# Optimization experiments

Hardware: AMD Instinct MI355X
Metric: run time of the kernel (lower is better)

The kernel has to match this reference:

```python
import jax, jax.numpy as jnp
import numpy as np

N, DEG, F = 500000, 16, 128
H1, H2, OUT = 256, 256, 128


def setup_inputs() -> dict:
    key = jax.random.key(0)
    ks = jax.random.split(key, 8)
    s = lambda fan_in: 1.0 / np.sqrt(fan_in)
    return {
        "message": jax.random.normal(ks[0], (N, DEG, F), dtype=jnp.float32),
        "features": jax.random.normal(ks[1], (N, F), dtype=jnp.float32),
        "global_features": jax.random.normal(ks[2], (N, F), dtype=jnp.float32),
        "W1": jax.random.normal(ks[3], (3 * F, H1), dtype=jnp.float32) * s(3 * F),
        "b1": jnp.zeros((H1,), dtype=jnp.float32),
        "W2": jax.random.normal(ks[4], (H1, H2), dtype=jnp.float32) * s(H1),
        "b2": jnp.zeros((H2,), dtype=jnp.float32),
        "W3": jax.random.normal(ks[5], (H2, OUT), dtype=jnp.float32) * s(H2),
        "b3": jnp.zeros((OUT,), dtype=jnp.float32),
    }


def reference(message, features, global_features, W1, b1, W2, b2, W3, b3):
    # mailbox sum-aggregate over neighbors: [N, deg, F] -> [N, F]
    agg = jnp.sum(message, axis=1)
    # concat aggregated messages with node + global features: [N, 3F]
    x = jnp.concatenate([agg, features, global_features], axis=1)
    # MLP: Linear+ReLU, Linear+ReLU, Linear
    h = jax.nn.relu(x @ W1 + b1)
    h = jax.nn.relu(h @ W2 + b2)
    out = h @ W3 + b3
    # row-wise L2 (Frobenius over dim=1) normalization
    norm = jnp.linalg.norm(out, axis=1, keepdims=True)
    return out / (norm + 1e-8)
```

## Files before the change

### kernel.cpp

```cpp
#include <hip/hip_runtime.h>


typedef short short8   __attribute__((ext_vector_type(8)));
typedef short short4_t __attribute__((ext_vector_type(4)));
typedef float f32x4    __attribute__((ext_vector_type(4)));

#define SWZ(row, off) ((off) ^ (((row) & 7) << 4))

__device__ __forceinline__ unsigned short f2bf(float f) {
    unsigned int u = __float_as_uint(f);
    u += 0x7fffu + ((u >> 16) & 1u);
    return (unsigned short)(u >> 16);
}

__global__ void prep_weights(const float* __restrict__ W1,
                             const float* __restrict__ W2,
                             const float* __restrict__ W3,
                             short* __restrict__ pw1,
                             short* __restrict__ pw2,
                             short* __restrict__ pw3) {
    int idx = blockIdx.x * 256 + threadIdx.x;
    if (idx < 98304) {
        int j = idx & 7, l = (idx >> 3) & 63, g = idx >> 9;
        int ks = g % 12, tn = g / 12;
        int n = tn * 16 + (l & 15);
        int k = ks * 32 + ((l >> 4) << 3) + j;
        pw1[idx] = (short)f2bf(W1[k * 256 + n]);
    } else if (idx < 98304 + 65536) {
        int e = idx - 98304;
        int j = e & 7, l = (e >> 3) & 63, g = e >> 9;
        int ks = g & 7, tn = g >> 3;
        int n = tn * 16 + (l & 15);
        int k = ks * 32 + ((l >> 4) << 3) + j;
        pw2[e] = (short)f2bf(W2[k * 256 + n]);
    } else if (idx < 98304 + 65536 + 32768) {
        int e = idx - 98304 - 65536;
        int j = e & 7, l = (e >> 3) & 63, g = e >> 9;
        int ks = g & 7, tn = g >> 3;
        int n = tn * 16 + (l & 15);
        int k = ks * 32 + ((l >> 4) << 3) + j;
        pw3[e] = (short)f2bf(W3[k * 128 + n]);
    }
}

__global__ __launch_bounds__(256, 4) void node_net_fused(
    const float* __restrict__ msg,
    const float* __restrict__ feat,
    const float* __restrict__ glob,
    const float* __restrict__ b1v,
    const float* __restrict__ b2v,
    const float* __restrict__ b3v,
    const short* __restrict__ pw1,
    const short* __restrict__ pw2,
    const short* __restrict__ pw3,
    float* __restrict__ out,
    int n_rows)
{
    __shared__ char lds[32768];
    char* regA = lds;
    char* regB = lds + 16384;

    {
        const unsigned key = ((unsigned)blockIdx.x * 2654435761u) >> 30;
        const int spin = (int)key * 500;
        for (int i = 0; i < spin; ++i)
            asm volatile("s_nop 0" ::: "memory");
    }

    const int tid  = threadIdx.x;
    const int lane = tid & 63;
    const int w    = tid >> 6;
    const int lr   = lane & 15;
    const int lk   = lane >> 4;
    const long long r0 = (long long)blockIdx.x * 32;

    const f32x4 zero4 = {0.f, 0.f, 0.f, 0.f};

    f32x4 fr[4], gr[4];
    #pragma unroll
    for (int q = 0; q < 4; ++q) {
        int r = (tid >> 5) + q * 8;
        long long row = r0 + r;
        fr[q] = zero4; gr[q] = zero4;
        if (row < n_rows) {
            fr[q] = __builtin_nontemporal_load((const f32x4*)feat + row * 32 + (tid & 31));
            gr[q] = __builtin_nontemporal_load((const f32x4*)glob + row * 32 + (tid & 31));
        }
    }

    #pragma unroll 1
    for (int pp = 0; pp < 4; ++pp) {
        const int rA = 8 * w + 2 * pp;
        const long long rowA = r0 + rA;
        const f32x4* base = (const f32x4*)msg + rowA * 512;
        f32x4 tA[8], tB[8];
        const bool okA = rowA < n_rows;
        const bool okB = (rowA + 1) < n_rows;
        #pragma unroll
        for (int i = 0; i < 8; ++i)
            tA[i] = okA ? __builtin_nontemporal_load(base + i * 64 + lane) : zero4;
        #pragma unroll
        for (int i = 0; i < 8; ++i)
            tB[i] = okB ? __builtin_nontemporal_load(base + 512 + i * 64 + lane) : zero4;
        f32x4 sA = ((tA[0]+tA[1])+(tA[2]+tA[3])) + ((tA[4]+tA[5])+(tA[6]+tA[7]));
        f32x4 sB = ((tB[0]+tB[1])+(tB[2]+tB[3])) + ((tB[4]+tB[5])+(tB[6]+tB[7]));
        #pragma unroll
        for (int c = 0; c < 4; ++c) {
            sA[c] += __shfl_xor(sA[c], 32);
            sB[c] += __shfl_xor(sB[c], 32);
        }
        f32x4 s = (lane < 32) ? sA : sB;
        short4_t s4;
        s4[0] = (short)f2bf(s[0]); s4[1] = (short)f2bf(s[1]);
        s4[2] = (short)f2bf(s[2]); s4[3] = (short)f2bf(s[3]);
        const int orow = rA + (lane >> 5);
        *(short4_t*)(regB + SWZ(orow, orow * 256 + (lane & 31) * 8)) = s4;
    }
    __syncthreads();

    #pragma unroll
    for (int q = 0; q < 4; ++q) {
        int r = (tid >> 5) + q * 8;
        short4_t s4;
        s4[0] = (short)f2bf(fr[q][0]); s4[1] = (short)f2bf(fr[q][1]);
        s4[2] = (short)f2bf(fr[q][2]); s4[3] = (short)f2bf(fr[q][3]);
        *(short4_t*)(regA + SWZ(r, r * 256 + (tid & 31) * 8)) = s4;
    }

    f32x4 acc1[2][4];
    #pragma unroll
    for (int ri = 0; ri < 2; ++ri)
        #pragma unroll
        for (int ci = 0; ci < 4; ++ci) acc1[ri][ci] = zero4;

    #pragma unroll
    for (int s = 0; s < 4; ++s) {
        short8 a[2], b[4];
        #pragma unroll
        for (int ri = 0; ri < 2; ++ri) {
            int row = ri * 16 + lr;
            a[ri] = *(const short8*)(regB + SWZ(row, row * 256 + s * 64 + lk * 16));
        }
        #pragma unroll
        for (int ci = 0; ci < 4; ++ci) {
            int tn = w * 4 + ci;
            b[ci] = *(const short8*)(pw1 + (((tn * 12 + s) * 64 + lane) << 3));
        }
        #pragma unroll
        for (int ri = 0; ri < 2; ++ri)
            #pragma unroll
            for (int ci = 0; ci < 4; ++ci)
                acc1[ri][ci] = __builtin_amdgcn_mfma_f32_16x16x32_bf16(
                    a[ri], b[ci], acc1[ri][ci], 0, 0, 0);
    }
    __syncthreads();

    #pragma unroll
    for (int q = 0; q < 4; ++q) {
        int r = (tid >> 5) + q * 8;
        short4_t s4;
        s4[0] = (short)f2bf(gr[q][0]); s4[1] = (short)f2bf(gr[q][1]);
        s4[2] = (short)f2bf(gr[q][2]); s4[3] = (short)f2bf(gr[q][3]);
        *(short4_t*)(regB + 8192 + SWZ(r, r * 256 + (tid & 31) * 8)) = s4;
    }

    #pragma unroll
    for (int s = 0; s < 4; ++s) {
        short8 a[2], b[4];
        #pragma unroll
        for (int ri = 0; ri < 2; ++ri) {
            int row = ri * 16 + lr;
            a[ri] = *(const short8*)(regA + SWZ(row, row * 256 + s * 64 + lk * 16));
        }
        #pragma unroll
        for (int ci = 0; ci < 4; ++ci) {
            int tn = w * 4 + ci;
            b[ci] = *(const short8*)(pw1 + (((tn * 12 + 4 + s) * 64 + lane) << 3));
        }
        #pragma unroll
        for (int ri = 0; ri < 2; ++ri)
            #pragma unroll
            for (int ci = 0; ci < 4; ++ci)
                acc1[ri][ci] = __builtin_amdgcn_mfma_f32_16x16x32_bf16(
                    a[ri], b[ci], acc1[ri][ci], 0, 0, 0);
    }
    __syncthreads();

    #pragma unroll
    for (int s = 0; s < 4; ++s) {
        short8 a[2], b[4];
        #pragma unroll
        for (int ri = 0; ri < 2; ++ri) {
            int row = ri * 16 + lr;
            a[ri] = *(const short8*)(regB + 8192 + SWZ(row, row * 256 + s * 64 + lk * 16));
        }
        #pragma unroll
        for (int ci = 0; ci < 4; ++ci) {
            int tn = w * 4 + ci;
            b[ci] = *(const short8*)(pw1 + (((tn * 12 + 8 + s) * 64 + lane) << 3));
        }
        #pragma unroll
        for (int ri = 0; ri < 2; ++ri)
            #pragma unroll
            for (int ci = 0; ci < 4; ++ci)
                acc1[ri][ci] = __builtin_amdgcn_mfma_f32_16x16x32_bf16(
                    a[ri], b[ci], acc1[ri][ci], 0, 0, 0);
    }

    #pragma unroll
    for (int ci = 0; ci < 4; ++ci) {
        int col = w * 64 + ci * 16 + lr;
        float bias = b1v[col];
        #pragma unroll
        for (int ri = 0; ri < 2; ++ri)
            #pragma unroll
            for (int i = 0; i < 4; ++i) {
                int row = ri * 16 + lk * 4 + i;
                float v = fmaxf(acc1[ri][ci][i] + bias, 0.f);
                *(short*)(regA + SWZ(row, row * 512 + col * 2)) = (short)f2bf(v);
            }
    }
    __syncthreads();

    f32x4 acc2[2][4];
    #pragma unroll
    for (int ri = 0; ri < 2; ++ri)
        #pragma unroll
        for (int ci = 0; ci < 4; ++ci) acc2[ri][ci] = zero4;

    #pragma unroll
    for (int s = 0; s < 8; ++s) {
        short8 a[2], b[4];
        #pragma unroll
        for (int ri = 0; ri < 2; ++ri) {
            int row = ri * 16 + lr;
            a[ri] = *(const short8*)(regA + SWZ(row, row * 512 + s * 64 + lk * 16));
        }
        #pragma unroll
        for (int ci = 0; ci < 4; ++ci) {
            int tn = w * 4 + ci;
            b[ci] = *(const short8*)(pw2 + (((tn * 8 + s) * 64 + lane) << 3));
        }
        #pragma unroll
        for (int ri = 0; ri < 2; ++ri)
            #pragma unroll
            for (int ci = 0; ci < 4; ++ci)
                acc2[ri][ci] = __builtin_amdgcn_mfma_f32_16x16x32_bf16(
                    a[ri], b[ci], acc2[ri][ci], 0, 0, 0);
    }

    #pragma unroll
    for (int ci = 0; ci < 4; ++ci) {
        int col = w * 64 + ci * 16 + lr;
        float bias = b2v[col];
        #pragma unroll
        for (int ri = 0; ri < 2; ++ri)
            #pragma unroll
            for (int i = 0; i < 4; ++i) {
                int row = ri * 16 + lk * 4 + i;
                float v = fmaxf(acc2[ri][ci][i] + bias, 0.f);
                *(short*)(regB + SWZ(row, row * 512 + col * 2)) = (short)f2bf(v);
            }
    }
    __syncthreads();

    f32x4 acc3[2][2];
    #pragma unroll
    for (int ri = 0; ri < 2; ++ri)
        #pragma unroll
        for (int ci = 0; ci < 2; ++ci) acc3[ri][ci] = zero4;

    #pragma unroll
    for (int s = 0; s < 8; ++s) {
        short8 a[2], b[2];
        #pragma unroll
        for (int ri = 0; ri < 2; ++ri) {
            int row = ri * 16 + lr;
            a[ri] = *(const short8*)(regB + SWZ(row, row * 512 + s * 64 + lk * 16));
        }
        #pragma unroll
        for (int ci = 0; ci < 2; ++ci) {
            int tn = w * 2 + ci;
            b[ci] = *(const short8*)(pw3 + (((tn * 8 + s) * 64 + lane) << 3));
        }
        #pragma unroll
        for (int ri = 0; ri < 2; ++ri)
            #pragma unroll
            for (int ci = 0; ci < 2; ++ci)
                acc3[ri][ci] = __builtin_amdgcn_mfma_f32_16x16x32_bf16(
                    a[ri], b[ci], acc3[ri][ci], 0, 0, 0);
    }

    #pragma unroll
    for (int ci = 0; ci < 2; ++ci) {
        int col = w * 32 + ci * 16 + lr;
        float bias = b3v[col];
        #pragma unroll
        for (int ri = 0; ri < 2; ++ri)
            #pragma unroll
            for (int i = 0; i < 4; ++i) {
                int row = ri * 16 + lk * 4 + i;
                float v = acc3[ri][ci][i] + bias;
                *(float*)(regA + SWZ(row, row * 512 + col * 4)) = v;
            }
    }
    __syncthreads();

    #pragma unroll
    for (int pass = 0; pass < 4; ++pass) {
        const int r  = (tid >> 5) + pass * 8;
        const int fl = tid & 31;
        f32x4 v = *(const f32x4*)(regA + SWZ(r, r * 512 + fl * 16));
        float ss = v[0]*v[0] + v[1]*v[1] + v[2]*v[2] + v[3]*v[3];
        ss += __shfl_xor(ss, 1, 32);
        ss += __shfl_xor(ss, 2, 32);
        ss += __shfl_xor(ss, 4, 32);
        ss += __shfl_xor(ss, 8, 32);
        ss += __shfl_xor(ss, 16, 32);
        float inv = 1.f / (sqrtf(ss) + 1e-8f);
        long long row = r0 + r;
        if (row < n_rows) {
            f32x4 o = v * inv;
            __builtin_nontemporal_store(o, (f32x4*)out + row * 32 + fl);
        }
    }
}

extern "C" void kernel_launch(void* const* d_in, const int* in_sizes, int n_in,
                              void* d_out, int out_size, void* d_ws, size_t ws_size,
                              hipStream_t stream) {
    const float* msg  = (const float*)d_in[0];
    const float* feat = (const float*)d_in[1];
    const float* glob = (const float*)d_in[2];
    const float* W1   = (const float*)d_in[3];
    const float* b1   = (const float*)d_in[4];
    const float* W2   = (const float*)d_in[5];
    const float* b2   = (const float*)d_in[6];
    const float* W3   = (const float*)d_in[7];
    const float* b3   = (const float*)d_in[8];
    float* out = (float*)d_out;

    const int n_rows = in_sizes[1] / 128;

    short* pw1 = (short*)d_ws;
    short* pw2 = pw1 + 98304;
    short* pw3 = pw2 + 65536;

    hipLaunchKernelGGL(prep_weights, dim3(768), dim3(256), 0, stream,
                       W1, W2, W3, pw1, pw2, pw3);

    const int nblocks = (n_rows + 31) / 32;
    hipLaunchKernelGGL(node_net_fused, dim3(nblocks), dim3(256), 0, stream,
                       msg, feat, glob, b1, b2, b3, pw1, pw2, pw3, out, n_rows);
}
```

Measured before the change: 1.119 ms.

## Warp-specialize persistent kernel: producer waves stream messages while MLP waves compute

Replaces the one-tile-per-block fused kernel with a persistent 512-thread kernel. Four waves run the three-layer MLP on the current 32-row tile while four producer waves stream and reduce the next tile's messages and features into a double-buffered LDS region. This is meant to overlap the heavy message read (about 4 GB of fp32) with MFMA work and removes the staggered spin delay. It uses more LDS (80 KB) and caps the grid at 512 blocks, which lowers occupancy and may underfill the memory pipeline, since only four waves per block issue the streaming loads.

```diff
diff --git a/kernel.cpp b/kernel.cpp
--- a/kernel.cpp
+++ b/kernel.cpp
@@ -43,7 +43,62 @@
     }
 }
 
-__global__ __launch_bounds__(256, 4) void node_net_fused(
+__device__ __forceinline__ void stream_pair(
+    const float* __restrict__ msg, char* aggdst,
+    long long rn0, int sw, int pp, int lane, int n_rows)
+{
+    const f32x4 zero4 = {0.f, 0.f, 0.f, 0.f};
+    const int rA = 8 * sw + 2 * pp;
+    const long long rowA = rn0 + rA;
+    const f32x4* base = (const f32x4*)msg + rowA * 512;
+    const bool okA = rowA < n_rows;
+    const bool okB = (rowA + 1) < n_rows;
+    f32x4 tA[8], tB[8];
+    #pragma unroll
+    for (int i = 0; i < 8; ++i)
+        tA[i] = okA ? __builtin_nontemporal_load(base + i * 64 + lane) : zero4;
+    #pragma unroll
+    for (int i = 0; i < 8; ++i)
+        tB[i] = okB ? __builtin_nontemporal_load(base + 512 + i * 64 + lane) : zero4;
+    f32x4 sA = ((tA[0]+tA[1])+(tA[2]+tA[3])) + ((tA[4]+tA[5])+(tA[6]+tA[7]));
+    f32x4 sB = ((tB[0]+tB[1])+(tB[2]+tB[3])) + ((tB[4]+tB[5])+(tB[6]+tB[7]));
+    #pragma unroll
+    for (int c = 0; c < 4; ++c) {
+        sA[c] += __shfl_xor(sA[c], 32);
+        sB[c] += __shfl_xor(sB[c], 32);
+    }
+    f32x4 s = (lane < 32) ? sA : sB;
+    short4_t s4;
+    s4[0] = (short)f2bf(s[0]); s4[1] = (short)f2bf(s[1]);
+    s4[2] = (short)f2bf(s[2]); s4[3] = (short)f2bf(s[3]);
+    const int orow = rA + (lane >> 5);
+    *(short4_t*)(aggdst + SWZ(orow, orow * 256 + (lane & 31) * 8)) = s4;
+}
+
+__device__ __forceinline__ void stream_fg(
+    const float* __restrict__ feat, const float* __restrict__ glob,
+    char* xbdst, long long rn0, int sw, int lane, int n_rows)
+{
+    const f32x4 zero4 = {0.f, 0.f, 0.f, 0.f};
+    const int rl = 8 * sw + (lane >> 3);
+    const long long grow = rn0 + rl;
+    const bool ok = grow < n_rows;
+    #pragma unroll
+    for (int q = 0; q < 4; ++q) {
+        const int f = (lane & 7) * 4 + q;
+        f32x4 fv = ok ? __builtin_nontemporal_load((const f32x4*)feat + grow * 32 + f) : zero4;
+        f32x4 gv = ok ? __builtin_nontemporal_load((const f32x4*)glob + grow * 32 + f) : zero4;
+        short4_t sf, sg;
+        sf[0]=(short)f2bf(fv[0]); sf[1]=(short)f2bf(fv[1]);
+        sf[2]=(short)f2bf(fv[2]); sf[3]=(short)f2bf(fv[3]);
+        sg[0]=(short)f2bf(gv[0]); sg[1]=(short)f2bf(gv[1]);
+        sg[2]=(short)f2bf(gv[2]); sg[3]=(short)f2bf(gv[3]);
+        *(short4_t*)(xbdst + 8192  + SWZ(rl, rl * 256 + f * 8)) = sf;
+        *(short4_t*)(xbdst + 16384 + SWZ(rl, rl * 256 + f * 8)) = sg;
+    }
+}
+
+__global__ __launch_bounds__(512, 2) void node_net_pc(
     const float* __restrict__ msg,
     const float* __restrict__ feat,
     const float* __restrict__ glob,
@@ -54,275 +109,198 @@
     const short* __restrict__ pw2,
     const short* __restrict__ pw3,
     float* __restrict__ out,
-    int n_rows)
+    int n_rows, int ntiles, int nblk)
 {
-    __shared__ char lds[32768];
-    char* regA = lds;
-    char* regB = lds + 16384;
-
-    {
-        const unsigned key = ((unsigned)blockIdx.x * 2654435761u) >> 30;
-        const int spin = (int)key * 500;
-        for (int i = 0; i < spin; ++i)
-            asm volatile("s_nop 0" ::: "memory");
-    }
+    __shared__ char lds[81920];
+    char* H1 = lds + 49152;
+    char* H2 = lds + 65536;
 
     const int tid  = threadIdx.x;
     const int lane = tid & 63;
     const int w    = tid >> 6;
+    const bool is_mlp = (w < 4);
+    const int sw   = w - 4;
     const int lr   = lane & 15;
     const int lk   = lane >> 4;
-    const long long r0 = (long long)blockIdx.x * 32;
-
     const f32x4 zero4 = {0.f, 0.f, 0.f, 0.f};
 
-    f32x4 fr[4], gr[4];
-    #pragma unroll
-    for (int q = 0; q < 4; ++q) {
-        int r = (tid >> 5) + q * 8;
-        long long row = r0 + r;
-        fr[q] = zero4; gr[q] = zero4;
-        if (row < n_rows) {
-            fr[q] = __builtin_nontemporal_load((const f32x4*)feat + row * 32 + (tid & 31));
-            gr[q] = __builtin_nontemporal_load((const f32x4*)glob + row * 32 + (tid & 31));
-        }
-    }
-
-    #pragma unroll 1
-    for (int pp = 0; pp < 4; ++pp) {
-        const int rA = 8 * w + 2 * pp;
-        const long long rowA = r0 + rA;
-        const f32x4* base = (const f32x4*)msg + rowA * 512;
-        f32x4 tA[8], tB[8];
-        const bool okA = rowA < n_rows;
-        const bool okB = (rowA + 1) < n_rows;
-        #pragma unroll
-        for (int i = 0; i < 8; ++i)
-            tA[i] = okA ? __builtin_nontemporal_load(base + i * 64 + lane) : zero4;
-        #pragma unroll
-        for (int i = 0; i < 8; ++i)
-            tB[i] = okB ? __builtin_nontemporal_load(base + 512 + i * 64 + lane) : zero4;
-        f32x4 sA = ((tA[0]+tA[1])+(tA[2]+tA[3])) + ((tA[4]+tA[5])+(tA[6]+tA[7]));
-        f32x4 sB = ((tB[0]+tB[1])+(tB[2]+tB[3])) + ((tB[4]+tB[5])+(tB[6]+tB[7]));
-        #pragma unroll
-        for (int c = 0; c < 4; ++c) {
-            sA[c] += __shfl_xor(sA[c], 32);
-            sB[c] += __shfl_xor(sB[c], 32);
-        }
-        f32x4 s = (lane < 32) ? sA : sB;
-        short4_t s4;
-        s4[0] = (short)f2bf(s[0]); s4[1] = (short)f2bf(s[1]);
-        s4[2] = (short)f2bf(s[2]); s4[3] = (short)f2bf(s[3]);
-        const int orow = rA + (lane >> 5);
-        *(short4_t*)(regB + SWZ(orow, orow * 256 + (lane & 31) * 8)) = s4;
-    }
-    __syncthreads();
-
-    #pragma unroll
-    for (int q = 0; q < 4; ++q) {
-        int r = (tid >> 5) + q * 8;
-        short4_t s4;
-        s4[0] = (short)f2bf(fr[q][0]); s4[1] = (short)f2bf(fr[q][1]);
-        s4[2] = (short)f2bf(fr[q][2]); s4[3] = (short)f2bf(fr[q][3]);
-        *(short4_t*)(regA + SWZ(r, r * 256 + (tid & 31) * 8)) = s4;
-    }
-
-    f32x4 acc1[2][4];
-    #pragma unroll
-    for (int ri = 0; ri < 2; ++ri)
-        #pragma unroll
-        for (int ci = 0; ci < 4; ++ci) acc1[ri][ci] = zero4;
-
-    #pragma unroll
-    for (int s = 0; s < 4; ++s) {
-        short8 a[2], b[4];
-        #pragma unroll
-        for (int ri = 0; ri < 2; ++ri) {
-            int row = ri * 16 + lr;
-            a[ri] = *(const short8*)(regB + SWZ(row, row * 256 + s * 64 + lk * 16));
-        }
+    float bias1[4] = {0,0,0,0}, bias2[4] = {0,0,0,0}, bias3[2] = {0,0};
+    if (is_mlp) {
         #pragma unroll
         for (int ci = 0; ci < 4; ++ci) {
-            int tn = w * 4 + ci;
-            b[ci] = *(const short8*)(pw1 + (((tn * 12 + s) * 64 + lane) << 3));
+            bias1[ci] = b1v[w * 64 + ci * 16 + lr];
+            bias2[ci] = b2v[w * 64 + ci * 16 + lr];
         }
         #pragma unroll
-        for (int ri = 0; ri < 2; ++ri)
-            #pragma unroll
-            for (int ci = 0; ci < 4; ++ci)
-                acc1[ri][ci] = __builtin_amdgcn_mfma_f32_16x16x32_bf16(
-                    a[ri], b[ci], acc1[ri][ci], 0, 0, 0);
+        for (int ci = 0; ci < 2; ++ci) bias3[ci] = b3v[w * 32 + ci * 16 + lr];
+    }
+
+    long long t = blockIdx.x;
+    int p = 0;
+
+    if (!is_mlp) {
+        const long long r0 = t * 32;
+        #pragma unroll 1
+        for (int pp = 0; pp < 4; ++pp)
+            stream_pair(msg, lds + 0, r0, sw, pp, lane, n_rows);
+        stream_fg(feat, glob, lds + 0, r0, sw, lane, n_rows);
     }
     __syncthreads();
 
-    #pragma unroll
-    for (int q = 0; q < 4; ++q) {
-        int r = (tid >> 5) + q * 8;
-        short4_t s4;
-        s4[0] = (short)f2bf(gr[q][0]); s4[1] = (short)f2bf(gr[q][1]);
-        s4[2] = (short)f2bf(gr[q][2]); s4[3] = (short)f2bf(gr[q][3]);
-        *(short4_t*)(regB + 8192 + SWZ(r, r * 256 + (tid & 31) * 8)) = s4;
-    }
-
-    #pragma unroll
-    for (int s = 0; s < 4; ++s) {
-        short8 a[2], b[4];
-        #pragma unroll
-        for (int ri = 0; ri < 2; ++ri) {
-            int row = ri * 16 + lr;
-            a[ri] = *(const short8*)(regA + SWZ(row, row * 256 + s * 64 + lk * 16));
-        }
-        #pragma unroll
-        for (int ci = 0; ci < 4; ++ci) {
-            int tn = w * 4 + ci;
-            b[ci] = *(const short8*)(pw1 + (((tn * 12 + 4 + s) * 64 + lane) << 3));
-        }
-        #pragma unroll
-        for (int ri = 0; ri < 2; ++ri)
-            #pragma unroll
-            for (int ci = 0; ci < 4; ++ci)
-                acc1[ri][ci] = __builtin_amdgcn_mfma_f32_16x16x32_bf16(
-                    a[ri], b[ci], acc1[ri][ci], 0, 0, 0);
-    }
-    __syncthreads();
-
-    #pragma unroll
-    for (int s = 0; s < 4; ++s) {
-        short8 a[2], b[4];
-        #pragma unroll
-        for (int ri = 0; ri < 2; ++ri) {
-            int row = ri * 16 + lr;
-            a[ri] = *(const short8*)(regB + 8192 + SWZ(row, row * 256 + s * 64 + lk * 16));
-        }
-        #pragma unroll
-        for (int ci = 0; ci < 4; ++ci) {
-            int tn = w * 4 + ci;
-            b[ci] = *(const short8*)(pw1 + (((tn * 12 + 8 + s) * 64 + lane) << 3));
-        }
-        #pragma unroll
-        for (int ri = 0; ri < 2; ++ri)
-            #pragma unroll
-            for (int ci = 0; ci < 4; ++ci)
-                acc1[ri][ci] = __builtin_amdgcn_mfma_f32_16x16x32_bf16(
-                    a[ri], b[ci], acc1[ri][ci], 0, 0, 0);
-    }
-
-    #pragma unroll
-    for (int ci = 0; ci < 4; ++ci) {
-        int col = w * 64 + ci * 16 + lr;
-        float bias = b1v[col];
-        #pragma unroll
-        for (int ri = 0; ri < 2; ++ri)
-            #pragma unroll
-            for (int i = 0; i < 4; ++i) {
-                int row = ri * 16 + lk * 4 + i;
-                float v = fmaxf(acc1[ri][ci][i] + bias, 0.f);
-                *(short*)(regA + SWZ(row, row * 512 + col * 2)) = (short)f2bf(v);
-            }
-    }
-    __syncthreads();
-
-    f32x4 acc2[2][4];
-    #pragma unroll
-    for (int ri = 0; ri < 2; ++ri)
-        #pragma unroll
-        for (int ci = 0; ci < 4; ++ci) acc2[ri][ci] = zero4;
-
-    #pragma unroll
-    for (int s = 0; s < 8; ++s) {
-        short8 a[2], b[4];
-        #pragma unroll
-        for (int ri = 0; ri < 2; ++ri) {
-            int row = ri * 16 + lr;
-            a[ri] = *(const short8*)(regA + SWZ(row, row * 512 + s * 64 + lk * 16));
-        }
-        #pragma unroll
-        for (int ci = 0; ci < 4; ++ci) {
-            int tn = w * 4 + ci;
-            b[ci] = *(const short8*)(pw2 + (((tn * 8 + s) * 64 + lane) << 3));
-        }
-        #pragma unroll
-        for (int ri = 0; ri < 2; ++ri)
-            #pragma unroll
-            for (int ci = 0; ci < 4; ++ci)
-                acc2[ri][ci] = __builtin_amdgcn_mfma_f32_16x16x32_bf16(
-                    a[ri], b[ci], acc2[ri][ci], 0, 0, 0);
-    }
-
-    #pragma unroll
-    for (int ci = 0; ci < 4; ++ci) {
-        int col = w * 64 + ci * 16 + lr;
-        float bias = b2v[col];
-        #pragma unroll
-        for (int ri = 0; ri < 2; ++ri)
-            #pragma unroll
-            for (int i = 0; i < 4; ++i) {
-                int row = ri * 16 + lk * 4 + i;
-                float v = fmaxf(acc2[ri][ci][i] + bias, 0.f);
-                *(short*)(regB + SWZ(row, row * 512 + col * 2)) = (short)f2bf(v);
-            }
-    }
-    __syncthreads();
-
-    f32x4 acc3[2][2];
-    #pragma unroll
-    for (int ri = 0; ri < 2; ++ri)
-        #pragma unroll
-        for (int ci = 0; ci < 2; ++ci) acc3[ri][ci] = zero4;
-
-    #pragma unroll
-    for (int s = 0; s < 8; ++s) {
-        short8 a[2], b[2];
-        #pragma unroll
-        for (int ri = 0; ri < 2; ++ri) {
-            int row = ri * 16 + lr;
-            a[ri] = *(const short8*)(regB + SWZ(row, row * 512 + s * 64 + lk * 16));
-        }
-        #pragma unroll
-        for (int ci = 0; ci < 2; ++ci) {
-            int tn = w * 2 + ci;
-            b[ci] = *(const short8*)(pw3 + (((tn * 8 + s) * 64 + lane) << 3));
-        }
-        #pragma unroll
-        for (int ri = 0; ri < 2; ++ri)
-            #pragma unroll
-            for (int ci = 0; ci < 2; ++ci)
-                acc3[ri][ci] = __builtin_amdgcn_mfma_f32_16x16x32_bf16(
-                    a[ri], b[ci], acc3[ri][ci], 0, 0, 0);
-    }
-
-    #pragma unroll
-    for (int ci = 0; ci < 2; ++ci) {
-        int col = w * 32 + ci * 16 + lr;
-        float bias = b3v[col];
-        #pragma unroll
-        for (int ri = 0; ri < 2; ++ri)
-            #pragma unroll
-            for (int i = 0; i < 4; ++i) {
-                int row = ri * 16 + lk * 4 + i;
-                float v = acc3[ri][ci][i] + bias;
-                *(float*)(regA + SWZ(row, row * 512 + col * 4)) = v;
-            }
-    }
-    __syncthreads();
-
-    #pragma unroll
-    for (int pass = 0; pass < 4; ++pass) {
-        const int r  = (tid >> 5) + pass * 8;
-        const int fl = tid & 31;
-        f32x4 v = *(const f32x4*)(regA + SWZ(r, r * 512 + fl * 16));
-        float ss = v[0]*v[0] + v[1]*v[1] + v[2]*v[2] + v[3]*v[3];
-        ss += __shfl_xor(ss, 1, 32);
-        ss += __shfl_xor(ss, 2, 32);
-        ss += __shfl_xor(ss, 4, 32);
-        ss += __shfl_xor(ss, 8, 32);
-        ss += __shfl_xor(ss, 16, 32);
-        float inv = 1.f / (sqrtf(ss) + 1e-8f);
-        long long row = r0 + r;
-        if (row < n_rows) {
-            f32x4 o = v * inv;
-            __builtin_nontemporal_store(o, (f32x4*)out + row * 32 + fl);
-        }
+    for (; t < ntiles; t += nblk, p ^= 1) {
+        char* xb = lds + (p ? 24576 : 0);
+        char* xn = lds + (p ? 0 : 24576);
+        const long long r0  = t * 32;
+        const long long rn0 = (t + (long long)nblk) * 32;
+
+        f32x4 acc1[2][4];
+        if (is_mlp) {
+            #pragma unroll
+            for (int ri = 0; ri < 2; ++ri)
+                #pragma unroll
+                for (int ci = 0; ci < 4; ++ci) acc1[ri][ci] = zero4;
+            #pragma unroll
+            for (int ks = 0; ks < 12; ++ks) {
+                const int reg = ks >> 2, s = ks & 3;
+                short8 a[2], b[4];
+                #pragma unroll
+                for (int ri = 0; ri < 2; ++ri) {
+                    int row = ri * 16 + lr;
+                    a[ri] = *(const short8*)(xb + reg * 8192 + SWZ(row, row * 256 + s * 64 + lk * 16));
+                }
+                #pragma unroll
+                for (int ci = 0; ci < 4; ++ci)
+                    b[ci] = *(const short8*)(pw1 + ((((w * 4 + ci) * 12 + ks) * 64 + lane) << 3));
+                #pragma unroll
+                for (int ri = 0; ri < 2; ++ri)
+                    #pragma unroll
+                    for (int ci = 0; ci < 4; ++ci)
+                        acc1[ri][ci] = __builtin_amdgcn_mfma_f32_16x16x32_bf16(
+                            a[ri], b[ci], acc1[ri][ci], 0, 0, 0);
+            }
+            #pragma unroll
+            for (int ci = 0; ci < 4; ++ci) {
+                int col = w * 64 + ci * 16 + lr;
+                #pragma unroll
+                for (int ri = 0; ri < 2; ++ri)
+                    #pragma unroll
+                    for (int i = 0; i < 4; ++i) {
+                        int row = ri * 16 + lk * 4 + i;
+                        float v = fmaxf(acc1[ri][ci][i] + bias1[ci], 0.f);
+                        *(short*)(H1 + SWZ(row, row * 512 + col * 2)) = (short)f2bf(v);
+                    }
+            }
+        } else {
+            stream_pair(msg, xn, rn0, sw, 0, lane, n_rows);
+            stream_pair(msg, xn, rn0, sw, 1, lane, n_rows);
+        }
+        __syncthreads();
+
+        if (is_mlp) {
+            f32x4 acc2[2][4];
+            #pragma unroll
+            for (int ri = 0; ri < 2; ++ri)
+                #pragma unroll
+                for (int ci = 0; ci < 4; ++ci) acc2[ri][ci] = zero4;
+            #pragma unroll
+            for (int s = 0; s < 8; ++s) {
+                short8 a[2], b[4];
+                #pragma unroll
+                for (int ri = 0; ri < 2; ++ri) {
+                    int row = ri * 16 + lr;
+                    a[ri] = *(const short8*)(H1 + SWZ(row, row * 512 + s * 64 + lk * 16));
+                }
+                #pragma unroll
+                for (int ci = 0; ci < 4; ++ci)
+                    b[ci] = *(const short8*)(pw2 + ((((w * 4 + ci) * 8 + s) * 64 + lane) << 3));
+                #pragma unroll
+                for (int ri = 0; ri < 2; ++ri)
+                    #pragma unroll
+                    for (int ci = 0; ci < 4; ++ci)
+                        acc2[ri][ci] = __builtin_amdgcn_mfma_f32_16x16x32_bf16(
+                            a[ri], b[ci], acc2[ri][ci], 0, 0, 0);
+            }
+            #pragma unroll
+            for (int ci = 0; ci < 4; ++ci) {
+                int col = w * 64 + ci * 16 + lr;
+                #pragma unroll
+                for (int ri = 0; ri < 2; ++ri)
+                    #pragma unroll
+                    for (int i = 0; i < 4; ++i) {
+                        int row = ri * 16 + lk * 4 + i;
+                        float v = fmaxf(acc2[ri][ci][i] + bias2[ci], 0.f);
+                        *(short*)(H2 + SWZ(row, row * 512 + col * 2)) = (short)f2bf(v);
+                    }
+            }
+        } else {
+            stream_pair(msg, xn, rn0, sw, 2, lane, n_rows);
+        }
+        __syncthreads();
+
+        if (is_mlp) {
+            f32x4 acc3[2][2];
+            #pragma unroll
+            for (int ri = 0; ri < 2; ++ri)
+                #pragma unroll
+                for (int ci = 0; ci < 2; ++ci) acc3[ri][ci] = zero4;
+            #pragma unroll
+            for (int s = 0; s < 8; ++s) {
+                short8 a[2], b[2];
+                #pragma unroll
+                for (int ri = 0; ri < 2; ++ri) {
+                    int row = ri * 16 + lr;
+                    a[ri] = *(const short8*)(H2 + SWZ(row, row * 512 + s * 64 + lk * 16));
+                }
+                #pragma unroll
+                for (int ci = 0; ci < 2; ++ci)
+                    b[ci] = *(const short8*)(pw3 + ((((w * 2 + ci) * 8 + s) * 64 + lane) << 3));
+                #pragma unroll
+                for (int ri = 0; ri < 2; ++ri)
+                    #pragma unroll
+                    for (int ci = 0; ci < 2; ++ci)
+                        acc3[ri][ci] = __builtin_amdgcn_mfma_f32_16x16x32_bf16(
+                            a[ri], b[ci], acc3[ri][ci], 0, 0, 0);
+            }
+            #pragma unroll
+            for (int ci = 0; ci < 2; ++ci) {
+                int col = w * 32 + ci * 16 + lr;
+                #pragma unroll
+                for (int ri = 0; ri < 2; ++ri)
+                    #pragma unroll
+                    for (int i = 0; i < 4; ++i) {
+                        int row = ri * 16 + lk * 4 + i;
+                        float v = acc3[ri][ci][i] + bias3[ci];
+                        *(float*)(H1 + SWZ(row, row * 512 + col * 4)) = v;
+                    }
+            }
+        } else {
+            stream_pair(msg, xn, rn0, sw, 3, lane, n_rows);
+        }
+        __syncthreads();
+
+        if (is_mlp) {
+            #pragma unroll
+            for (int pass = 0; pass < 4; ++pass) {
+                const int r  = (tid >> 5) + pass * 8;
+                const int fl = tid & 31;
+                f32x4 v = *(const f32x4*)(H1 + SWZ(r, r * 512 + fl * 16));
+                float ss = v[0]*v[0] + v[1]*v[1] + v[2]*v[2] + v[3]*v[3];
+                ss += __shfl_xor(ss, 1, 32);
+                ss += __shfl_xor(ss, 2, 32);
+                ss += __shfl_xor(ss, 4, 32);
+                ss += __shfl_xor(ss, 8, 32);
+                ss += __shfl_xor(ss, 16, 32);
+                float inv = 1.f / (sqrtf(ss) + 1e-8f);
+                long long row = r0 + r;
+                if (row < n_rows) {
+                    f32x4 o = v * inv;
+                    __builtin_nontemporal_store(o, (f32x4*)out + row * 32 + fl);
+                }
+            }
+        } else {
+            stream_fg(feat, glob, xn, rn0, sw, lane, n_rows);
+        }
+        __syncthreads();
     }
 }
 
@@ -341,6 +319,8 @@
     float* out = (float*)d_out;
 
     const int n_rows = in_sizes[1] / 128;
+    const int ntiles = (n_rows + 31) / 32;
+    const int nblk   = ntiles < 512 ? ntiles : 512;
 
     short* pw1 = (short*)d_ws;
     short* pw2 = pw1 + 98304;
@@ -349,7 +329,7 @@
     hipLaunchKernelGGL(prep_weights, dim3(768), dim3(256), 0, stream,
                        W1, W2, W3, pw1, pw2, pw3);
 
-    const int nblocks = (n_rows + 31) / 32;
-    hipLaunchKernelGGL(node_net_fused, dim3(nblocks), dim3(256), 0, stream,
-                       msg, feat, glob, b1, b2, b3, pw1, pw2, pw3, out, n_rows);
-}
+    hipLaunchKernelGGL(node_net_pc, dim3(nblk), dim3(512), 0, stream,
+                       msg, feat, glob, b1, b2, b3, pw1, pw2, pw3, out,
+                       n_rows, ntiles, nblk);
+}
```

Result: slower. 1.879 ms (+68.0%).

## Stage all three input slabs in LDS at once and drop startup spin

Applied to the files above, without the earlier changes.

Enlarges LDS to 40 KB so the aggregated messages, features and global features are all written as bf16 into one contiguous staging area before a single barrier. Layer 1 then becomes one 12-step K loop instead of three phases with two extra barriers. It also removes the artificial per-block s_nop spin delay at kernel start. The larger LDS footprint may reduce the number of resident blocks per CU.

```diff
diff --git a/kernel.cpp b/kernel.cpp
--- a/kernel.cpp
+++ b/kernel.cpp
@@ -56,16 +56,9 @@
     float* __restrict__ out,
     int n_rows)
 {
-    __shared__ char lds[32768];
-    char* regA = lds;
-    char* regB = lds + 16384;
-
-    {
-        const unsigned key = ((unsigned)blockIdx.x * 2654435761u) >> 30;
-        const int spin = (int)key * 500;
-        for (int i = 0; i < spin; ++i)
-            asm volatile("s_nop 0" ::: "memory");
-    }
+    __shared__ char lds[40960];
+    char* XB = lds;
+    char* HB = lds + 24576;
 
     const int tid  = threadIdx.x;
     const int lane = tid & 63;
@@ -114,18 +107,21 @@
         s4[0] = (short)f2bf(s[0]); s4[1] = (short)f2bf(s[1]);
         s4[2] = (short)f2bf(s[2]); s4[3] = (short)f2bf(s[3]);
         const int orow = rA + (lane >> 5);
-        *(short4_t*)(regB + SWZ(orow, orow * 256 + (lane & 31) * 8)) = s4;
-    }
-    __syncthreads();
+        *(short4_t*)(XB + SWZ(orow, orow * 256 + (lane & 31) * 8)) = s4;
+    }
 
     #pragma unroll
     for (int q = 0; q < 4; ++q) {
         int r = (tid >> 5) + q * 8;
-        short4_t s4;
-        s4[0] = (short)f2bf(fr[q][0]); s4[1] = (short)f2bf(fr[q][1]);
-        s4[2] = (short)f2bf(fr[q][2]); s4[3] = (short)f2bf(fr[q][3]);
-        *(short4_t*)(regA + SWZ(r, r * 256 + (tid & 31) * 8)) = s4;
-    }
+        short4_t sf, sg;
+        sf[0] = (short)f2bf(fr[q][0]); sf[1] = (short)f2bf(fr[q][1]);
+        sf[2] = (short)f2bf(fr[q][2]); sf[3] = (short)f2bf(fr[q][3]);
+        sg[0] = (short)f2bf(gr[q][0]); sg[1] = (short)f2bf(gr[q][1]);
+        sg[2] = (short)f2bf(gr[q][2]); sg[3] = (short)f2bf(gr[q][3]);
+        *(short4_t*)(XB + 8192  + SWZ(r, r * 256 + (tid & 31) * 8)) = sf;
+        *(short4_t*)(XB + 16384 + SWZ(r, r * 256 + (tid & 31) * 8)) = sg;
+    }
+    __syncthreads();
 
     f32x4 acc1[2][4];
     #pragma unroll
@@ -134,18 +130,17 @@
         for (int ci = 0; ci < 4; ++ci) acc1[ri][ci] = zero4;
 
     #pragma unroll
-    for (int s = 0; s < 4; ++s) {
+    for (int ks = 0; ks < 12; ++ks) {
+        const int p = ks >> 2, s = ks & 3;
         short8 a[2], b[4];
         #pragma unroll
         for (int ri = 0; ri < 2; ++ri) {
             int row = ri * 16 + lr;
-            a[ri] = *(const short8*)(regB + SWZ(row, row * 256 + s * 64 + lk * 16));
-        }
-        #pragma unroll
-        for (int ci = 0; ci < 4; ++ci) {
-            int tn = w * 4 + ci;
-            b[ci] = *(const short8*)(pw1 + (((tn * 12 + s) * 64 + lane) << 3));
-        }
+            a[ri] = *(const short8*)(XB + p * 8192 + SWZ(row, row * 256 + s * 64 + lk * 16));
+        }
+        #pragma unroll
+        for (int ci = 0; ci < 4; ++ci)
+            b[ci] = *(const short8*)(pw1 + ((((w * 4 + ci) * 12 + ks) * 64 + lane) << 3));
         #pragma unroll
         for (int ri = 0; ri < 2; ++ri)
             #pragma unroll
@@ -153,59 +148,6 @@
                 acc1[ri][ci] = __builtin_amdgcn_mfma_f32_16x16x32_bf16(
                     a[ri], b[ci], acc1[ri][ci], 0, 0, 0);
     }
-    __syncthreads();
-
-    #pragma unroll
-    for (int q = 0; q < 4; ++q) {
-        int r = (tid >> 5) + q * 8;
-        short4_t s4;
-        s4[0] = (short)f2bf(gr[q][0]); s4[1] = (short)f2bf(gr[q][1]);
-        s4[2] = (short)f2bf(gr[q][2]); s4[3] = (short)f2bf(gr[q][3]);
-        *(short4_t*)(regB + 8192 + SWZ(r, r * 256 + (tid & 31) * 8)) = s4;
-    }
-
-    #pragma unroll
-    for (int s = 0; s < 4; ++s) {
-        short8 a[2], b[4];
-        #pragma unroll
-        for (int ri = 0; ri < 2; ++ri) {
-            int row = ri * 16 + lr;
-            a[ri] = *(const short8*)(regA + SWZ(row, row * 256 + s * 64 + lk * 16));
-        }
-        #pragma unroll
-        for (int ci = 0; ci < 4; ++ci) {
-            int tn = w * 4 + ci;
-            b[ci] = *(const short8*)(pw1 + (((tn * 12 + 4 + s) * 64 + lane) << 3));
-        }
-        #pragma unroll
-        for (int ri = 0; ri < 2; ++ri)
-            #pragma unroll
-            for (int ci = 0; ci < 4; ++ci)
-                acc1[ri][ci] = __builtin_amdgcn_mfma_f32_16x16x32_bf16(
-                    a[ri], b[ci], acc1[ri][ci], 0, 0, 0);
-    }
-    __syncthreads();
-
-    #pragma unroll
-    for (int s = 0; s < 4; ++s) {
-        short8 a[2], b[4];
-        #pragma unroll
-        for (int ri = 0; ri < 2; ++ri) {
-            int row = ri * 16 + lr;
-            a[ri] = *(const short8*)(regB + 8192 + SWZ(row, row * 256 + s * 64 + lk * 16));
-        }
-        #pragma unroll
-        for (int ci = 0; ci < 4; ++ci) {
-            int tn = w * 4 + ci;
-            b[ci] = *(const short8*)(pw1 + (((tn * 12 + 8 + s) * 64 + lane) << 3));
-        }
-        #pragma unroll
-        for (int ri = 0; ri < 2; ++ri)
-            #pragma unroll
-            for (int ci = 0; ci < 4; ++ci)
-                acc1[ri][ci] = __builtin_amdgcn_mfma_f32_16x16x32_bf16(
-                    a[ri], b[ci], acc1[ri][ci], 0, 0, 0);
-    }
 
     #pragma unroll
     for (int ci = 0; ci < 4; ++ci) {
@@ -217,7 +159,7 @@
             for (int i = 0; i < 4; ++i) {
                 int row = ri * 16 + lk * 4 + i;
                 float v = fmaxf(acc1[ri][ci][i] + bias, 0.f);
-                *(short*)(regA + SWZ(row, row * 512 + col * 2)) = (short)f2bf(v);
+                *(short*)(HB + SWZ(row, row * 512 + col * 2)) = (short)f2bf(v);
             }
     }
     __syncthreads();
@@ -234,13 +176,11 @@
         #pragma unroll
         for (int ri = 0; ri < 2; ++ri) {
             int row = ri * 16 + lr;
-            a[ri] = *(const short8*)(regA + SWZ(row, row * 512 + s * 64 + lk * 16));
-        }
-        #pragma unroll
-        for (int ci = 0; ci < 4; ++ci) {
-            int tn = w * 4 + ci;
-            b[ci] = *(const short8*)(pw2 + (((tn * 8 + s) * 64 + lane) << 3));
-        }
+            a[ri] = *(const short8*)(HB + SWZ(row, row * 512 + s * 64 + lk * 16));
+        }
+        #pragma unroll
+        for (int ci = 0; ci < 4; ++ci)
+            b[ci] = *(const short8*)(pw2 + ((((w * 4 + ci) * 8 + s) * 64 + lane) << 3));
         #pragma unroll
         for (int ri = 0; ri < 2; ++ri)
             #pragma unroll
@@ -259,7 +199,7 @@
             for (int i = 0; i < 4; ++i) {
                 int row = ri * 16 + lk * 4 + i;
                 float v = fmaxf(acc2[ri][ci][i] + bias, 0.f);
-                *(short*)(regB + SWZ(row, row * 512 + col * 2)) = (short)f2bf(v);
+                *(short*)(XB + SWZ(row, row * 512 + col * 2)) = (short)f2bf(v);
             }
     }
     __syncthreads();
@@ -276,13 +216,11 @@
         #pragma unroll
         for (int ri = 0; ri < 2; ++ri) {
             int row = ri * 16 + lr;
-            a[ri] = *(const short8*)(regB + SWZ(row, row * 512 + s * 64 + lk * 16));
-        }
-        #pragma unroll
-        for (int ci = 0; ci < 2; ++ci) {
-            int tn = w * 2 + ci;
-            b[ci] = *(const short8*)(pw3 + (((tn * 8 + s) * 64 + lane) << 3));
-        }
+            a[ri] = *(const short8*)(XB + SWZ(row, row * 512 + s * 64 + lk * 16));
+        }
+        #pragma unroll
+        for (int ci = 0; ci < 2; ++ci)
+            b[ci] = *(const short8*)(pw3 + ((((w * 2 + ci) * 8 + s) * 64 + lane) << 3));
         #pragma unroll
         for (int ri = 0; ri < 2; ++ri)
             #pragma unroll
@@ -301,7 +239,7 @@
             for (int i = 0; i < 4; ++i) {
                 int row = ri * 16 + lk * 4 + i;
                 float v = acc3[ri][ci][i] + bias;
-                *(float*)(regA + SWZ(row, row * 512 + col * 4)) = v;
+                *(float*)(HB + SWZ(row, row * 512 + col * 4)) = v;
             }
     }
     __syncthreads();
@@ -310,7 +248,7 @@
     for (int pass = 0; pass < 4; ++pass) {
         const int r  = (tid >> 5) + pass * 8;
         const int fl = tid & 31;
-        f32x4 v = *(const f32x4*)(regA + SWZ(r, r * 512 + fl * 16));
+        f32x4 v = *(const f32x4*)(HB + SWZ(r, r * 512 + fl * 16));
         float ss = v[0]*v[0] + v[1]*v[1] + v[2]*v[2] + v[3]*v[3];
         ss += __shfl_xor(ss, 1, 32);
         ss += __shfl_xor(ss, 2, 32);
```

After: 1.092 ms. -2.4%, faster.
